# Performance work log

Measured on AMD Instinct MI355X. Metric: run time of the kernel, lower is better.

## Reference

```python
import jax, jax.numpy as jnp
import numpy as np

N_NODES = 50000
N_GRAPHS = 4
N_EDGES = 800000
D_IN = 128
D_OUT = 128


def setup_inputs() -> dict:
    key = jax.random.key(0)
    ks = jax.random.split(key, 7)
    x = jax.random.normal(ks[0], (N_NODES, D_IN), dtype=jnp.float32)
    edge_rows = jax.random.randint(ks[1], (N_GRAPHS, N_EDGES), 0, N_NODES, dtype=jnp.int32)
    edge_cols = jax.random.randint(ks[2], (N_GRAPHS, N_EDGES), 0, N_NODES, dtype=jnp.int32)
    edge_vals = jax.random.uniform(ks[3], (N_GRAPHS, N_EDGES), dtype=jnp.float32)
    W = jax.random.normal(ks[4], (N_GRAPHS, D_IN, D_OUT), dtype=jnp.float32) * (1.0 / np.sqrt(D_IN))
    mixing_weight = jax.random.uniform(ks[5], (N_GRAPHS, 1), dtype=jnp.float32, minval=-0.25, maxval=0.25)
    bias = jax.random.uniform(ks[6], (D_OUT,), dtype=jnp.float32, minval=-0.25, maxval=0.25)
    return {"x": x, "edge_rows": edge_rows, "edge_cols": edge_cols,
            "edge_vals": edge_vals, "W": W, "mixing_weight": mixing_weight, "bias": bias}


def _spmm(rows, cols, vals, dense):
    # sparse [N,N] (COO) @ dense [N,F] -> [N,F]
    gathered = dense[cols] * vals[:, None]          # [E, F]
    return jax.ops.segment_sum(gathered, rows, num_segments=N_NODES)


def reference(x, edge_rows, edge_cols, edge_vals, W, mixing_weight, bias):
    # Per-graph linear projection: [L, N, F_out]
    pre_sup = jnp.einsum('nd,ldf->lnf', x, W)
    # Per-graph spmm via vmap over graphs
    graph_outputs = jax.vmap(_spmm)(edge_rows, edge_cols, edge_vals, pre_sup)  # [L, N, F_out]
    # Weighted mix across graphs (tensordot + squeeze in torch)
    out = jnp.einsum('l,lnf->nf', mixing_weight[:, 0], graph_outputs)
    return out + bias
```

## Files before the change

### kernel.cpp

```cpp
#include <hip/hip_runtime.h>


constexpr int N = 50000;
constexpr int E = 800000;
constexpr int D = 128;
constexpr int L = 4;
constexpr int BSH = 4;
constexpr int NB = N >> BSH;
constexpr int NCHK = 100;
constexpr int CHUNK = E / NCHK;
constexpr int CAP = 1024;

typedef __attribute__((ext_vector_type(8))) short bf16x8;
typedef __attribute__((ext_vector_type(4))) float f32x4;
union U4B8 { uint4 u; bf16x8 b; };

__device__ inline unsigned bf16rne(unsigned u) {
    return (u + 0x7FFFu + ((u >> 16) & 1u)) >> 16;
}

__global__ __launch_bounds__(256) void cvt_x_kernel(
    const float* __restrict__ x, unsigned* __restrict__ xb)
{
    int i = blockIdx.x * 256 + threadIdx.x;
    int row = i >> 6, j = i & 63;
    int q = j >> 4, fl = j & 15;
    float2 v = *reinterpret_cast<const float2*>(x + (size_t)row * D + q * 32 + fl * 2);
    xb[((size_t)q * N + row) * 16 + fl] =
        bf16rne(__float_as_uint(v.x)) | (bf16rne(__float_as_uint(v.y)) << 16);
}

__global__ __launch_bounds__(256) void cvt_w_kernel(
    const float* __restrict__ W, const float* __restrict__ mix,
    unsigned* __restrict__ WbT)
{
    int idx = blockIdx.x * 256 + threadIdx.x;
    int f = idx & 127, dp = (idx >> 7) & 63, l = idx >> 13;
    float m = mix[l];
    float a = m * W[((size_t)l * D + 2 * dp) * D + f];
    float b = m * W[((size_t)l * D + 2 * dp + 1) * D + f];
    WbT[((size_t)l * D + f) * 64 + dp] =
        bf16rne(__float_as_uint(a)) | (bf16rne(__float_as_uint(b)) << 16);
}

__global__ __launch_bounds__(256) void fill2_kernel(
    const int* __restrict__ edge_rows,
    const int* __restrict__ edge_cols,
    const float* __restrict__ edge_vals,
    unsigned short* __restrict__ pcnt,
    unsigned short* __restrict__ chunkoff,
    unsigned* __restrict__ cvT,
    unsigned char* __restrict__ rlT)
{
    __shared__ int cnt[NB];
    __shared__ int psum[256];
    __shared__ unsigned lcv[CHUNK];
    __shared__ unsigned char lrl[CHUNK];
    const int blk = blockIdx.x, g = blockIdx.y, tid = threadIdx.x;

    for (int i = tid; i < NB; i += 256) cnt[i] = 0;
    __syncthreads();

    const size_t eoff = (size_t)g * E + (size_t)blk * CHUNK;
    const int* rows = edge_rows + eoff;
    const int* cols = edge_cols + eoff;
    const float* vals = edge_vals + eoff;

    for (int i = tid; i < CHUNK; i += 256)
        atomicAdd(&cnt[rows[i] >> BSH], 1);
    __syncthreads();

    unsigned short* pc = pcnt + ((size_t)g * NCHK + blk) * NB;
    for (int i = tid; i < NB; i += 256) pc[i] = (unsigned short)cnt[i];
    __syncthreads();

    constexpr int CB = (NB + 255) / 256;
    const int base = tid * CB;
    int s = 0;
#pragma unroll
    for (int j = 0; j < CB; ++j) {
        int idx = base + j;
        if (idx < NB) s += cnt[idx];
    }
    psum[tid] = s;
    __syncthreads();
    for (int off = 1; off < 256; off <<= 1) {
        int v = (tid >= off) ? psum[tid - off] : 0;
        __syncthreads();
        psum[tid] += v;
        __syncthreads();
    }
    int carry = (tid == 0) ? 0 : psum[tid - 1];
#pragma unroll
    for (int j = 0; j < CB; ++j) {
        int idx = base + j;
        if (idx < NB) {
            int c = cnt[idx];
            cnt[idx] = carry;
            carry += c;
        }
    }
    __syncthreads();

    unsigned short* co = chunkoff + ((size_t)g * NCHK + blk) * NB;
    for (int i = tid; i < NB; i += 256) co[i] = (unsigned short)cnt[i];
    __syncthreads();

    for (int i = tid; i < CHUNK; i += 256) {
        int r = rows[i];
        int b = r >> BSH;
        int pos = atomicAdd(&cnt[b], 1);
        lcv[pos] = (unsigned)cols[i] | (bf16rne(__float_as_uint(vals[i])) << 16);
        lrl[pos] = (unsigned char)(r & 15);
    }
    __syncthreads();

    unsigned* cw = cvT + eoff;
    unsigned char* rw = rlT + eoff;
    for (int i = tid; i < CHUNK; i += 256) cw[i] = lcv[i];
    for (int i = tid * 4; i < CHUNK; i += 1024)
        *reinterpret_cast<uint*>(rw + i) = *reinterpret_cast<const uint*>(lrl + i);
}

__global__ __launch_bounds__(256) void scan1_kernel(
    unsigned short* __restrict__ pcnt, int* __restrict__ bstart)
{
    const int b = blockIdx.x * 256 + threadIdx.x;
    const int g = blockIdx.y;
    if (b >= NB) return;
    unsigned run = 0;
    unsigned short* p = pcnt + (size_t)g * NCHK * NB + b;
    for (int blk = 0; blk < NCHK; ++blk) {
        unsigned v = p[(size_t)blk * NB];
        p[(size_t)blk * NB] = (unsigned short)run;
        run += v;
    }
    bstart[(size_t)g * (NB + 1) + b] = (int)run;
}

__global__ __launch_bounds__(1024) void scan2_kernel(int* __restrict__ bstart)
{
    __shared__ int sums[1024];
    int* bs = bstart + (size_t)blockIdx.x * (NB + 1);
    const int t = threadIdx.x;
    int tv[4];
    int s = 0;
#pragma unroll
    for (int i = 0; i < 4; ++i) {
        int idx = t * 4 + i;
        tv[i] = (idx < NB) ? bs[idx] : 0;
        s += tv[i];
    }
    sums[t] = s;
    __syncthreads();
    for (int off = 1; off < 1024; off <<= 1) {
        int v = (t >= off) ? sums[t - off] : 0;
        __syncthreads();
        sums[t] += v;
        __syncthreads();
    }
    int ex = (t == 0) ? 0 : sums[t - 1];
#pragma unroll
    for (int i = 0; i < 4; ++i) {
        int idx = t * 4 + i;
        if (idx < NB) { bs[idx] = ex; ex += tv[i]; }
    }
    if (t == 0) bs[NB] = E;
}

__global__ __launch_bounds__(256) void sort2_kernel(
    const unsigned* __restrict__ cvT,
    const unsigned char* __restrict__ rlT,
    const unsigned short* __restrict__ pcnt,
    const unsigned short* __restrict__ chunkoff,
    const int* __restrict__ bstart,
    unsigned* __restrict__ cv,
    int* __restrict__ rowptr)
{
    __shared__ unsigned su_cv[CAP], ss_cv[CAP];
    __shared__ unsigned char su_rl[CAP];
    __shared__ int rc[17], rcur[16];
    const int b = blockIdx.x, g = blockIdx.y, tid = threadIdx.x;
    const int beg = bstart[(size_t)g * (NB + 1) + b];
    const int tot = bstart[(size_t)g * (NB + 1) + b + 1] - beg;
    const int cnt = tot < CAP ? tot : CAP;
    int* rp = rowptr + (size_t)g * (N + 1);
    if (b == 0 && tid == 0) rp[N] = E;
    if (tid < 17) rc[tid] = 0;

    if (tid < NCHK) {
        const int c = tid;
        const size_t pbase = ((size_t)g * NCHK + c) * NB + b;
        int off = pcnt[pbase];
        int nxt = (c == NCHK - 1) ? tot : (int)pcnt[pbase + NB];
        int len = nxt - off;
        const size_t wbase = (size_t)g * E + (size_t)c * CHUNK + chunkoff[pbase];
        const unsigned* cw = cvT + wbase;
        const unsigned char* rw = rlT + wbase;
        for (int i = 0; i < len; ++i) {
            int p = off + i;
            if (p < CAP) { su_cv[p] = cw[i]; su_rl[p] = rw[i]; }
        }
    }
    __syncthreads();

    for (int i = tid; i < cnt; i += 256) atomicAdd(&rc[su_rl[i] + 1], 1);
    __syncthreads();
    if (tid == 0) {
        int run = 0;
#pragma unroll
        for (int r = 1; r <= 16; ++r) { run += rc[r]; rc[r] = run; }
    }
    __syncthreads();
    if (tid < 16) {
        rcur[tid] = rc[tid];
        rp[b * 16 + tid] = beg + rc[tid];
    }
    __syncthreads();
    for (int i = tid; i < cnt; i += 256) {
        int p = atomicAdd(&rcur[su_rl[i]], 1);
        ss_cv[p] = su_cv[i];
    }
    __syncthreads();
    unsigned* cvg = cv + (size_t)g * E;
    for (int i = tid; i < cnt; i += 256) cvg[beg + i] = ss_cv[i];
}

__global__ __launch_bounds__(256) void gather_kernel(
    const unsigned* __restrict__ xb,
    const unsigned* __restrict__ cv,
    const int* __restrict__ rowptr,
    unsigned* __restrict__ y,
    int q)
{
    const int tid = threadIdx.x;
    const int lane = tid & 63;
    const int wave = tid >> 6;
    const int sub = lane >> 4;
    const int fl = lane & 15;
    const int subbase = lane & 48;
    const int row = blockIdx.x * 16 + wave * 4 + sub;
    const int l = blockIdx.y;

    const unsigned* xq = xb + (size_t)q * N * 16;
    const unsigned* cvg = cv + (size_t)l * E;
    const int* rp = rowptr + (size_t)l * (N + 1);

    const int beg = rp[row], end = rp[row + 1];
    float accx = 0.f, accy = 0.f;

    for (int base = beg; base < end; base += 16) {
        const int cnt = end - base;
        unsigned cvr = (fl < cnt) ? cvg[base + fl] : 0u;
#pragma unroll
        for (int k = 0; k < 16; k += 4) {
            unsigned c0 = __shfl(cvr, subbase + k + 0);
            unsigned c1 = __shfl(cvr, subbase + k + 1);
            unsigned c2 = __shfl(cvr, subbase + k + 2);
            unsigned c3 = __shfl(cvr, subbase + k + 3);
            unsigned x0 = xq[(size_t)(c0 & 0xFFFFu) * 16 + fl];
            unsigned x1 = xq[(size_t)(c1 & 0xFFFFu) * 16 + fl];
            unsigned x2 = xq[(size_t)(c2 & 0xFFFFu) * 16 + fl];
            unsigned x3 = xq[(size_t)(c3 & 0xFFFFu) * 16 + fl];
            float v0 = __uint_as_float(c0 & 0xFFFF0000u);
            float v1 = __uint_as_float(c1 & 0xFFFF0000u);
            float v2 = __uint_as_float(c2 & 0xFFFF0000u);
            float v3 = __uint_as_float(c3 & 0xFFFF0000u);
            accx = fmaf(v0, __uint_as_float(x0 << 16), accx);
            accy = fmaf(v0, __uint_as_float(x0 & 0xFFFF0000u), accy);
            accx = fmaf(v1, __uint_as_float(x1 << 16), accx);
            accy = fmaf(v1, __uint_as_float(x1 & 0xFFFF0000u), accy);
            accx = fmaf(v2, __uint_as_float(x2 << 16), accx);
            accy = fmaf(v2, __uint_as_float(x2 & 0xFFFF0000u), accy);
            accx = fmaf(v3, __uint_as_float(x3 << 16), accx);
            accy = fmaf(v3, __uint_as_float(x3 & 0xFFFF0000u), accy);
        }
    }

    y[((size_t)l * N + row) * 16 + fl] =
        bf16rne(__float_as_uint(accx)) | (bf16rne(__float_as_uint(accy)) << 16);
}

__global__ __launch_bounds__(256) void gemm_mfma_kernel(
    const unsigned* __restrict__ y,
    const unsigned* __restrict__ WbT,
    const float* __restrict__ bias,
    float* __restrict__ out,
    int q)
{
    const int tid = threadIdx.x;
    const int lane = tid & 63, w = tid >> 6;
    const int r0 = blockIdx.x * 32;
    const int rows16 = (w & 1) * 16;
    const int fbase = (w >> 1) * 64;
    const int lrow = lane & 15, kgrp = lane >> 4;

    f32x4 acc[4] = {};
    const int arow = r0 + rows16 + lrow;

#pragma unroll
    for (int l = 0; l < L; ++l) {
        U4B8 a;
        a.u = (arow < N)
            ? *reinterpret_cast<const uint4*>(y + ((size_t)l * N + arow) * 16 + kgrp * 4)
            : make_uint4(0u, 0u, 0u, 0u);
#pragma unroll
        for (int t = 0; t < 4; ++t) {
            const int f = fbase + t * 16 + lrow;
            U4B8 bb;
            bb.u = *reinterpret_cast<const uint4*>(
                WbT + ((size_t)l * D + f) * 64 + q * 16 + kgrp * 4);
            acc[t] = __builtin_amdgcn_mfma_f32_16x16x32_bf16(a.b, bb.b, acc[t], 0, 0, 0);
        }
    }

#pragma unroll
    for (int t = 0; t < 4; ++t) {
        const int f = fbase + t * 16 + lrow;
#pragma unroll
        for (int i = 0; i < 4; ++i) {
            int row = r0 + rows16 + kgrp * 4 + i;
            if (row < N) {
                float* p = out + (size_t)row * D + f;
                float v = acc[t][i];
                *p = (q == 0) ? v + bias[f] : *p + v;
            }
        }
    }
}

extern "C" void kernel_launch(void* const* d_in, const int* in_sizes, int n_in,
                              void* d_out, int out_size, void* d_ws, size_t ws_size,
                              hipStream_t stream)
{
    const float* x         = (const float*)d_in[0];
    const int*   edge_rows = (const int*)d_in[1];
    const int*   edge_cols = (const int*)d_in[2];
    const float* edge_vals = (const float*)d_in[3];
    const float* W         = (const float*)d_in[4];
    const float* mix       = (const float*)d_in[5];
    const float* bias      = (const float*)d_in[6];
    float* out = (float*)d_out;

    unsigned*       cvT      = (unsigned*)d_ws;
    unsigned char*  rlT      = (unsigned char*)(cvT + (size_t)L * E);
    unsigned short* pcnt     = (unsigned short*)(rlT + (size_t)L * E);
    unsigned short* chunkoff = pcnt + (size_t)L * NCHK * NB;
    int*            bstart   = (int*)(chunkoff + (size_t)L * NCHK * NB);
    int*            rowptr   = bstart + (size_t)L * (NB + 1);
    unsigned*       cv       = (unsigned*)(rowptr + (size_t)L * (N + 1));
    unsigned*       xb       = cv + (size_t)L * E;
    unsigned*       WbT      = xb + (size_t)4 * N * 16;
    unsigned*       y        = cvT;

    cvt_x_kernel<<<(N * 64) / 256, 256, 0, stream>>>(x, xb);
    cvt_w_kernel<<<(L * D * 64) / 256, 256, 0, stream>>>(W, mix, WbT);
    fill2_kernel<<<dim3(NCHK, L), 256, 0, stream>>>(edge_rows, edge_cols, edge_vals,
                                                    pcnt, chunkoff, cvT, rlT);
    scan1_kernel<<<dim3((NB + 255) / 256, L), 256, 0, stream>>>(pcnt, bstart);
    scan2_kernel<<<L, 1024, 0, stream>>>(bstart);
    sort2_kernel<<<dim3(NB, L), 256, 0, stream>>>(cvT, rlT, pcnt, chunkoff, bstart,
                                                  cv, rowptr);

    for (int q = 0; q < 4; ++q) {
        gather_kernel<<<dim3(N / 16, L), 256, 0, stream>>>(xb, cv, rowptr, y, q);
        gemm_mfma_kernel<<<(N + 31) / 32, 256, 0, stream>>>(y, WbT, bias, out, q);
    }
}
```

Baseline: 316.4 us.

## Fuse gather and MFMA GEMM per row tile; split fill into hist and scatter

Merges the per-graph sparse gather and the bf16 MFMA projection into one kernel. Each block gathers 16 rows for every graph, stages them in shared memory and feeds them straight into MFMA, so the intermediate y buffer is never written to or read from global memory and half the launches go away. The fill kernel is split into a histogram kernel and a scatter kernel, and the scatter packs two 16-bit cursors per shared word. This frees shared memory in the scatter and may raise occupancy. In exchange the fused kernel loops over graphs serially with block barriers, has fewer blocks (no graph dimension), and launches an extra kernel for the split fill.

```diff
diff --git a/kernel.cpp b/kernel.cpp
--- a/kernel.cpp
+++ b/kernel.cpp
@@ -43,29 +43,19 @@
         bf16rne(__float_as_uint(a)) | (bf16rne(__float_as_uint(b)) << 16);
 }
 
-__global__ __launch_bounds__(256) void fill2_kernel(
+__global__ __launch_bounds__(256) void hist_kernel(
     const int* __restrict__ edge_rows,
-    const int* __restrict__ edge_cols,
-    const float* __restrict__ edge_vals,
     unsigned short* __restrict__ pcnt,
-    unsigned short* __restrict__ chunkoff,
-    unsigned* __restrict__ cvT,
-    unsigned char* __restrict__ rlT)
+    unsigned short* __restrict__ chunkoff)
 {
     __shared__ int cnt[NB];
     __shared__ int psum[256];
-    __shared__ unsigned lcv[CHUNK];
-    __shared__ unsigned char lrl[CHUNK];
     const int blk = blockIdx.x, g = blockIdx.y, tid = threadIdx.x;
 
     for (int i = tid; i < NB; i += 256) cnt[i] = 0;
     __syncthreads();
 
-    const size_t eoff = (size_t)g * E + (size_t)blk * CHUNK;
-    const int* rows = edge_rows + eoff;
-    const int* cols = edge_cols + eoff;
-    const float* vals = edge_vals + eoff;
-
+    const int* rows = edge_rows + (size_t)g * E + (size_t)blk * CHUNK;
     for (int i = tid; i < CHUNK; i += 256)
         atomicAdd(&cnt[rows[i] >> BSH], 1);
     __syncthreads();
@@ -104,12 +94,39 @@
 
     unsigned short* co = chunkoff + ((size_t)g * NCHK + blk) * NB;
     for (int i = tid; i < NB; i += 256) co[i] = (unsigned short)cnt[i];
-    __syncthreads();
+}
+
+__global__ __launch_bounds__(256) void scatter_kernel(
+    const int* __restrict__ edge_rows,
+    const int* __restrict__ edge_cols,
+    const float* __restrict__ edge_vals,
+    const unsigned short* __restrict__ chunkoff,
+    unsigned* __restrict__ cvT,
+    unsigned char* __restrict__ rlT)
+{
+    __shared__ unsigned cur[(NB + 1) / 2];
+    __shared__ unsigned lcv[CHUNK];
+    __shared__ unsigned char lrl[CHUNK];
+    const int blk = blockIdx.x, g = blockIdx.y, tid = threadIdx.x;
+
+    const unsigned short* co = chunkoff + ((size_t)g * NCHK + blk) * NB;
+    for (int i = tid; i < (NB + 1) / 2; i += 256) {
+        unsigned lo = co[2 * i];
+        unsigned hi = (2 * i + 1 < NB) ? co[2 * i + 1] : 0u;
+        cur[i] = lo | (hi << 16);
+    }
+    __syncthreads();
+
+    const size_t eoff = (size_t)g * E + (size_t)blk * CHUNK;
+    const int* rows = edge_rows + eoff;
+    const int* cols = edge_cols + eoff;
+    const float* vals = edge_vals + eoff;
 
     for (int i = tid; i < CHUNK; i += 256) {
         int r = rows[i];
         int b = r >> BSH;
-        int pos = atomicAdd(&cnt[b], 1);
+        unsigned old = atomicAdd(&cur[b >> 1], (b & 1) ? 0x10000u : 1u);
+        int pos = (old >> ((b & 1) * 16)) & 0xFFFFu;
         lcv[pos] = (unsigned)cols[i] | (bf16rne(__float_as_uint(vals[i])) << 16);
         lrl[pos] = (unsigned char)(r & 15);
     }
@@ -226,105 +243,90 @@
     for (int i = tid; i < cnt; i += 256) cvg[beg + i] = ss_cv[i];
 }
 
-__global__ __launch_bounds__(256) void gather_kernel(
+__global__ __launch_bounds__(256) void fused_kernel(
     const unsigned* __restrict__ xb,
     const unsigned* __restrict__ cv,
     const int* __restrict__ rowptr,
-    unsigned* __restrict__ y,
+    const unsigned* __restrict__ WbT,
+    const float* __restrict__ bias,
+    float* __restrict__ out,
     int q)
 {
+    __shared__ unsigned tile[16][16];
+
     const int tid = threadIdx.x;
     const int lane = tid & 63;
     const int wave = tid >> 6;
     const int sub = lane >> 4;
     const int fl = lane & 15;
     const int subbase = lane & 48;
-    const int row = blockIdx.x * 16 + wave * 4 + sub;
-    const int l = blockIdx.y;
+    const int trow = wave * 4 + sub;
+    const int row = blockIdx.x * 16 + trow;
+    const int lrow = lane & 15, kgrp = lane >> 4;
 
     const unsigned* xq = xb + (size_t)q * N * 16;
-    const unsigned* cvg = cv + (size_t)l * E;
-    const int* rp = rowptr + (size_t)l * (N + 1);
-
-    const int beg = rp[row], end = rp[row + 1];
-    float accx = 0.f, accy = 0.f;
-
-    for (int base = beg; base < end; base += 16) {
-        const int cnt = end - base;
-        unsigned cvr = (fl < cnt) ? cvg[base + fl] : 0u;
-#pragma unroll
-        for (int k = 0; k < 16; k += 4) {
-            unsigned c0 = __shfl(cvr, subbase + k + 0);
-            unsigned c1 = __shfl(cvr, subbase + k + 1);
-            unsigned c2 = __shfl(cvr, subbase + k + 2);
-            unsigned c3 = __shfl(cvr, subbase + k + 3);
-            unsigned x0 = xq[(size_t)(c0 & 0xFFFFu) * 16 + fl];
-            unsigned x1 = xq[(size_t)(c1 & 0xFFFFu) * 16 + fl];
-            unsigned x2 = xq[(size_t)(c2 & 0xFFFFu) * 16 + fl];
-            unsigned x3 = xq[(size_t)(c3 & 0xFFFFu) * 16 + fl];
-            float v0 = __uint_as_float(c0 & 0xFFFF0000u);
-            float v1 = __uint_as_float(c1 & 0xFFFF0000u);
-            float v2 = __uint_as_float(c2 & 0xFFFF0000u);
-            float v3 = __uint_as_float(c3 & 0xFFFF0000u);
-            accx = fmaf(v0, __uint_as_float(x0 << 16), accx);
-            accy = fmaf(v0, __uint_as_float(x0 & 0xFFFF0000u), accy);
-            accx = fmaf(v1, __uint_as_float(x1 << 16), accx);
-            accy = fmaf(v1, __uint_as_float(x1 & 0xFFFF0000u), accy);
-            accx = fmaf(v2, __uint_as_float(x2 << 16), accx);
-            accy = fmaf(v2, __uint_as_float(x2 & 0xFFFF0000u), accy);
-            accx = fmaf(v3, __uint_as_float(x3 << 16), accx);
-            accy = fmaf(v3, __uint_as_float(x3 & 0xFFFF0000u), accy);
-        }
-    }
-
-    y[((size_t)l * N + row) * 16 + fl] =
-        bf16rne(__float_as_uint(accx)) | (bf16rne(__float_as_uint(accy)) << 16);
-}
-
-__global__ __launch_bounds__(256) void gemm_mfma_kernel(
-    const unsigned* __restrict__ y,
-    const unsigned* __restrict__ WbT,
-    const float* __restrict__ bias,
-    float* __restrict__ out,
-    int q)
-{
-    const int tid = threadIdx.x;
-    const int lane = tid & 63, w = tid >> 6;
-    const int r0 = blockIdx.x * 32;
-    const int rows16 = (w & 1) * 16;
-    const int fbase = (w >> 1) * 64;
-    const int lrow = lane & 15, kgrp = lane >> 4;
-
-    f32x4 acc[4] = {};
-    const int arow = r0 + rows16 + lrow;
-
-#pragma unroll
+
+    f32x4 acc[2] = {};
+
     for (int l = 0; l < L; ++l) {
+        const unsigned* cvg = cv + (size_t)l * E;
+        const int* rp = rowptr + (size_t)l * (N + 1);
+        const int beg = rp[row], end = rp[row + 1];
+        float accx = 0.f, accy = 0.f;
+
+        for (int base = beg; base < end; base += 16) {
+            const int cnt = end - base;
+            unsigned cvr = (fl < cnt) ? cvg[base + fl] : 0u;
+#pragma unroll
+            for (int k = 0; k < 16; k += 4) {
+                unsigned c0 = __shfl(cvr, subbase + k + 0);
+                unsigned c1 = __shfl(cvr, subbase + k + 1);
+                unsigned c2 = __shfl(cvr, subbase + k + 2);
+                unsigned c3 = __shfl(cvr, subbase + k + 3);
+                unsigned x0 = xq[(size_t)(c0 & 0xFFFFu) * 16 + fl];
+                unsigned x1 = xq[(size_t)(c1 & 0xFFFFu) * 16 + fl];
+                unsigned x2 = xq[(size_t)(c2 & 0xFFFFu) * 16 + fl];
+                unsigned x3 = xq[(size_t)(c3 & 0xFFFFu) * 16 + fl];
+                float v0 = __uint_as_float(c0 & 0xFFFF0000u);
+                float v1 = __uint_as_float(c1 & 0xFFFF0000u);
+                float v2 = __uint_as_float(c2 & 0xFFFF0000u);
+                float v3 = __uint_as_float(c3 & 0xFFFF0000u);
+                accx = fmaf(v0, __uint_as_float(x0 << 16), accx);
+                accy = fmaf(v0, __uint_as_float(x0 & 0xFFFF0000u), accy);
+                accx = fmaf(v1, __uint_as_float(x1 << 16), accx);
+                accy = fmaf(v1, __uint_as_float(x1 & 0xFFFF0000u), accy);
+                accx = fmaf(v2, __uint_as_float(x2 << 16), accx);
+                accy = fmaf(v2, __uint_as_float(x2 & 0xFFFF0000u), accy);
+                accx = fmaf(v3, __uint_as_float(x3 << 16), accx);
+                accy = fmaf(v3, __uint_as_float(x3 & 0xFFFF0000u), accy);
+            }
+        }
+        tile[trow][fl] = bf16rne(__float_as_uint(accx)) |
+                         (bf16rne(__float_as_uint(accy)) << 16);
+        __syncthreads();
+
         U4B8 a;
-        a.u = (arow < N)
-            ? *reinterpret_cast<const uint4*>(y + ((size_t)l * N + arow) * 16 + kgrp * 4)
-            : make_uint4(0u, 0u, 0u, 0u);
-#pragma unroll
-        for (int t = 0; t < 4; ++t) {
-            const int f = fbase + t * 16 + lrow;
+        a.u = *reinterpret_cast<const uint4*>(&tile[lrow][kgrp * 4]);
+#pragma unroll
+        for (int t = 0; t < 2; ++t) {
+            const int f = wave * 32 + t * 16 + lrow;
             U4B8 bb;
             bb.u = *reinterpret_cast<const uint4*>(
                 WbT + ((size_t)l * D + f) * 64 + q * 16 + kgrp * 4);
             acc[t] = __builtin_amdgcn_mfma_f32_16x16x32_bf16(a.b, bb.b, acc[t], 0, 0, 0);
         }
-    }
-
-#pragma unroll
-    for (int t = 0; t < 4; ++t) {
-        const int f = fbase + t * 16 + lrow;
+        __syncthreads();
+    }
+
+#pragma unroll
+    for (int t = 0; t < 2; ++t) {
+        const int f = wave * 32 + t * 16 + lrow;
 #pragma unroll
         for (int i = 0; i < 4; ++i) {
-            int row = r0 + rows16 + kgrp * 4 + i;
-            if (row < N) {
-                float* p = out + (size_t)row * D + f;
-                float v = acc[t][i];
-                *p = (q == 0) ? v + bias[f] : *p + v;
-            }
+            int orow = blockIdx.x * 16 + kgrp * 4 + i;
+            float* p = out + (size_t)orow * D + f;
+            float v = acc[t][i];
+            *p = (q == 0) ? v + bias[f] : *p + v;
         }
     }
 }
@@ -351,19 +353,17 @@
     unsigned*       cv       = (unsigned*)(rowptr + (size_t)L * (N + 1));
     unsigned*       xb       = cv + (size_t)L * E;
     unsigned*       WbT      = xb + (size_t)4 * N * 16;
-    unsigned*       y        = cvT;
 
     cvt_x_kernel<<<(N * 64) / 256, 256, 0, stream>>>(x, xb);
     cvt_w_kernel<<<(L * D * 64) / 256, 256, 0, stream>>>(W, mix, WbT);
-    fill2_kernel<<<dim3(NCHK, L), 256, 0, stream>>>(edge_rows, edge_cols, edge_vals,
-                                                    pcnt, chunkoff, cvT, rlT);
+    hist_kernel<<<dim3(NCHK, L), 256, 0, stream>>>(edge_rows, pcnt, chunkoff);
+    scatter_kernel<<<dim3(NCHK, L), 256, 0, stream>>>(edge_rows, edge_cols,
+                                                      edge_vals, chunkoff, cvT, rlT);
     scan1_kernel<<<dim3((NB + 255) / 256, L), 256, 0, stream>>>(pcnt, bstart);
     scan2_kernel<<<L, 1024, 0, stream>>>(bstart);
     sort2_kernel<<<dim3(NB, L), 256, 0, stream>>>(cvT, rlT, pcnt, chunkoff, bstart,
                                                   cv, rowptr);
 
-    for (int q = 0; q < 4; ++q) {
-        gather_kernel<<<dim3(N / 16, L), 256, 0, stream>>>(xb, cv, rowptr, y, q);
-        gemm_mfma_kernel<<<(N + 31) / 32, 256, 0, stream>>>(y, WbT, bias, out, q);
-    }
-}
+    for (int q = 0; q < 4; ++q)
+        fused_kernel<<<N / 16, 256, 0, stream>>>(xb, cv, rowptr, WbT, bias, out, q);
+}
```

Result: faster. 303.9 us (-4.0%).
